# Kernel tuning notes

Measured on AMD Instinct MI355X. Metric: run time of the kernel, lower is better.

The kernel has to match this reference:

```python
import jax, jax.numpy as jnp
import numpy as np

A = -0.75  # bicubic kernel coefficient (matches torch/TF bicubic)

def _cubic_weights(t):
    """Cubic-convolution weights for the 4 taps at offsets -1,0,1,2; t in [0,1)."""
    def w_in(s):   # |s| <= 1
        return ((A + 2.0) * s - (A + 3.0)) * s * s + 1.0
    def w_out(s):  # 1 < |s| < 2
        return ((A * s - 5.0 * A) * s + 8.0 * A) * s - 4.0 * A
    return jnp.stack([w_out(t + 1.0), w_in(t), w_in(1.0 - t), w_out(2.0 - t)], axis=-1)

def setup_inputs() -> dict:
    key = jax.random.key(0)
    k1, k2 = jax.random.split(key)
    B, Hf, Wf, C = 8, 160, 160, 64
    H, W = 1280, 1280
    x = jax.random.normal(k1, (B, Hf, Wf, C), dtype=jnp.float32)
    # keypoint positions in original-image pixel coords [0, W-1] x [0, H-1]
    u = jax.random.uniform(k2, (B, 4096, 2), dtype=jnp.float32)
    pos = u * jnp.array([W - 1, H - 1], dtype=jnp.float32)
    return {"x": x, "pos": pos, "H": H, "W": W}

def reference(x, pos, H, W):
    """Bicubic grid_sample at sparse positions; align_corners=False, zeros padding.
    x: [B,Hf,Wf,C], pos: [B,N,2] (x,y) in original HxW pixel coords -> [B,N,C]."""
    B, Hf, Wf, C = x.shape
    # normalize to [-1,1] using the ORIGINAL resolution (H, W)
    gx = 2.0 * pos[..., 0] / (W - 1) - 1.0
    gy = 2.0 * pos[..., 1] / (H - 1) - 1.0
    # unnormalize to feature-map coords (align_corners=False)
    ix = ((gx + 1.0) * Wf - 1.0) * 0.5
    iy = ((gy + 1.0) * Hf - 1.0) * 0.5
    fx = jnp.floor(ix); fy = jnp.floor(iy)
    tx = ix - fx; ty = iy - fy
    offs = jnp.arange(-1, 3, dtype=jnp.int32)            # 4 taps
    xi = fx.astype(jnp.int32)[..., None] + offs           # [B,N,4]
    yi = fy.astype(jnp.int32)[..., None] + offs           # [B,N,4]
    wx = _cubic_weights(tx)                                # [B,N,4]
    wy = _cubic_weights(ty)                                # [B,N,4]
    # zeros padding: mask out-of-bounds taps
    vx = (xi >= 0) & (xi < Wf)
    vy = (yi >= 0) & (yi < Hf)
    xc = jnp.clip(xi, 0, Wf - 1)
    yc = jnp.clip(yi, 0, Hf - 1)
    lin = yc[:, :, :, None] * Wf + xc[:, :, None, :]       # [B,N,4,4] (i=y tap, j=x tap)
    xflat = x.reshape(B, Hf * Wf, C)
    vals = jax.vmap(lambda xb, ib: xb[ib])(xflat, lin)     # [B,N,4,4,C]
    m = (vy[:, :, :, None] & vx[:, :, None, :]).astype(x.dtype)
    vals = vals * m[..., None]
    return jnp.einsum('bnijc,bni,bnj->bnc', vals, wy, wx)  # [B,N,C]
```

## Files before the change

kernel.cpp:

```cpp
#include <hip/hip_runtime.h>
#include <hip/hip_bf16.h>

constexpr int B  = 8;
constexpr int Hf = 160;
constexpr int Wf = 160;
constexpr int C  = 64;
constexpr int N  = 4096;
constexpr int NXCD = 8;

typedef float f32x4 __attribute__((ext_vector_type(4)));
typedef float f32x2 __attribute__((ext_vector_type(2)));

__device__ __forceinline__ void cubic_weights(float t, float w[4]) {
    const float A = -0.75f;
    float s;
    s = t + 1.0f;
    w[0] = ((A * s - 5.0f * A) * s + 8.0f * A) * s - 4.0f * A;
    s = t;
    w[1] = ((A + 2.0f) * s - (A + 3.0f)) * s * s + 1.0f;
    s = 1.0f - t;
    w[2] = ((A + 2.0f) * s - (A + 3.0f)) * s * s + 1.0f;
    s = 2.0f - t;
    w[3] = ((A * s - 5.0f * A) * s + 8.0f * A) * s - 4.0f * A;
}

__global__ __launch_bounds__(256)
void interp_sparse_bicubic(const float* __restrict__ x,
                           const float* __restrict__ pos,
                           const int* __restrict__ Hp,
                           const int* __restrict__ Wp,
                           float* __restrict__ out) {
    int blk  = blockIdx.x;
    int b    = blk & (NXCD - 1);
    int slot = blk >> 3;
    int q    = threadIdx.x & 15;
    int pib  = threadIdx.x >> 4;
    int n    = slot * 16 + pib;
    int pnt  = b * N + n;

    f32x2 p = *reinterpret_cast<const f32x2*>(pos + (size_t)pnt * 2);
    float Wo = (float)Wp[0];
    float Ho = (float)Hp[0];

    float gx = 2.0f * p.x / (Wo - 1.0f) - 1.0f;
    float gy = 2.0f * p.y / (Ho - 1.0f) - 1.0f;
    float ix = ((gx + 1.0f) * (float)Wf - 1.0f) * 0.5f;
    float iy = ((gy + 1.0f) * (float)Hf - 1.0f) * 0.5f;

    float fx = floorf(ix), fy = floorf(iy);
    float tx = ix - fx,    ty = iy - fy;
    int x0 = (int)fx, y0 = (int)fy;

    float wx[4], wy[4];
    cubic_weights(tx, wx);
    cubic_weights(ty, wy);

    int yc[4], xc[4];
    #pragma unroll
    for (int i = 0; i < 4; ++i) {
        int yi = y0 - 1 + i;
        wy[i] = (yi >= 0 && yi < Hf) ? wy[i] : 0.0f;
        yc[i] = min(max(yi, 0), Hf - 1);
        int xj = x0 - 1 + i;
        wx[i] = (xj >= 0 && xj < Wf) ? wx[i] : 0.0f;
        xc[i] = min(max(xj, 0), Wf - 1);
    }

    const float* xb = x + (size_t)b * (Hf * Wf * C) + q * 4;

    f32x4 v[4][4];
    #pragma unroll
    for (int i = 0; i < 4; ++i) {
        const float* row = xb + (size_t)yc[i] * (Wf * C);
        #pragma unroll
        for (int j = 0; j < 4; ++j) {
            v[i][j] = *reinterpret_cast<const f32x4*>(row + (size_t)xc[j] * C);
        }
    }

    f32x4 acc = {0.f, 0.f, 0.f, 0.f};
    #pragma unroll
    for (int i = 0; i < 4; ++i) {
        #pragma unroll
        for (int j = 0; j < 4; ++j) {
            float w = wy[i] * wx[j];
            acc.x = fmaf(w, v[i][j].x, acc.x);
            acc.y = fmaf(w, v[i][j].y, acc.y);
            acc.z = fmaf(w, v[i][j].z, acc.z);
            acc.w = fmaf(w, v[i][j].w, acc.w);
        }
    }

    f32x4* op = reinterpret_cast<f32x4*>(out + (size_t)pnt * C + q * 4);
    __builtin_nontemporal_store(acc, op);
}

extern "C" void kernel_launch(void* const* d_in, const int* in_sizes, int n_in,
                              void* d_out, int out_size, void* d_ws, size_t ws_size,
                              hipStream_t stream) {
    const float* x   = (const float*)d_in[0];
    const float* pos = (const float*)d_in[1];
    const int*   Hp  = (const int*)d_in[2];
    const int*   Wp  = (const int*)d_in[3];
    float* out = (float*)d_out;

    int grid = B * (N / 16);
    interp_sparse_bicubic<<<grid, 256, 0, stream>>>(x, pos, Hp, Wp, out);
}
```

Baseline: 14.76 us.

## Bin keypoints into spatial tiles so blocks share cached feature neighborhoods

Adds a pre-pass that buckets each keypoint by its 13x13 feature-map tile, using atomic counters in the workspace and an overflow list for crowded bins. The interpolation kernel then processes one bin per block, so the points a block handles read overlapping 4x4 neighborhoods and get better cache reuse. This costs an extra memset and an extra kernel launch, uneven per-block work, and gather-indexed reads of pos and writes of out. If the workspace is too small, the original direct kernel is used instead.

Result: slower. 27.01 us (+83.0%).

```diff
diff --git a/kernel.cpp b/kernel.cpp
--- a/kernel.cpp
+++ b/kernel.cpp
@@ -7,6 +7,15 @@
 constexpr int C  = 64;
 constexpr int N  = 4096;
 constexpr int NXCD = 8;
+
+constexpr int TILE = 13;
+constexpr int TPS  = 13;
+constexpr int BINS = TPS * TPS;
+constexpr int CAP  = 64;
+constexpr int OBLK = 64;
+constexpr int CNTS = BINS + 1;
+
+constexpr size_t WS_NEED = (size_t)(B * CNTS + B * BINS * CAP + B * N) * 4;
 
 typedef float f32x4 __attribute__((ext_vector_type(4)));
 typedef float f32x2 __attribute__((ext_vector_type(2)));
@@ -24,23 +33,11 @@
     w[3] = ((A * s - 5.0f * A) * s + 8.0f * A) * s - 4.0f * A;
 }
 
-__global__ __launch_bounds__(256)
-void interp_sparse_bicubic(const float* __restrict__ x,
-                           const float* __restrict__ pos,
-                           const int* __restrict__ Hp,
-                           const int* __restrict__ Wp,
-                           float* __restrict__ out) {
-    int blk  = blockIdx.x;
-    int b    = blk & (NXCD - 1);
-    int slot = blk >> 3;
-    int q    = threadIdx.x & 15;
-    int pib  = threadIdx.x >> 4;
-    int n    = slot * 16 + pib;
-    int pnt  = b * N + n;
-
+__device__ __forceinline__ void eval_point(const float* __restrict__ xb,
+                                           const float* __restrict__ pos,
+                                           float* __restrict__ out,
+                                           int pnt, int q, float Wo, float Ho) {
     f32x2 p = *reinterpret_cast<const f32x2*>(pos + (size_t)pnt * 2);
-    float Wo = (float)Wp[0];
-    float Ho = (float)Hp[0];
 
     float gx = 2.0f * p.x / (Wo - 1.0f) - 1.0f;
     float gy = 2.0f * p.y / (Ho - 1.0f) - 1.0f;
@@ -66,16 +63,13 @@
         xc[i] = min(max(xj, 0), Wf - 1);
     }
 
-    const float* xb = x + (size_t)b * (Hf * Wf * C) + q * 4;
-
     f32x4 v[4][4];
     #pragma unroll
     for (int i = 0; i < 4; ++i) {
         const float* row = xb + (size_t)yc[i] * (Wf * C);
         #pragma unroll
-        for (int j = 0; j < 4; ++j) {
+        for (int j = 0; j < 4; ++j)
             v[i][j] = *reinterpret_cast<const f32x4*>(row + (size_t)xc[j] * C);
-        }
     }
 
     f32x4 acc = {0.f, 0.f, 0.f, 0.f};
@@ -95,6 +89,92 @@
     __builtin_nontemporal_store(acc, op);
 }
 
+__global__ __launch_bounds__(256)
+void bin_points(const float* __restrict__ pos, const int* __restrict__ Hp,
+                const int* __restrict__ Wp, int* __restrict__ ws) {
+    int pid = blockIdx.x * blockDim.x + threadIdx.x;
+    if (pid >= B * N) return;
+    int b = pid / N, n = pid - b * N;
+
+    f32x2 p = *reinterpret_cast<const f32x2*>(pos + (size_t)pid * 2);
+    float Wo = (float)Wp[0], Ho = (float)Hp[0];
+    float gx = 2.0f * p.x / (Wo - 1.0f) - 1.0f;
+    float gy = 2.0f * p.y / (Ho - 1.0f) - 1.0f;
+    float ix = ((gx + 1.0f) * (float)Wf - 1.0f) * 0.5f;
+    float iy = ((gy + 1.0f) * (float)Hf - 1.0f) * 0.5f;
+    int x0 = min(max((int)floorf(ix), 0), Wf - 1);
+    int y0 = min(max((int)floorf(iy), 0), Hf - 1);
+    int bin = (y0 / TILE) * TPS + (x0 / TILE);
+
+    int* cnt    = ws;
+    int* bucket = ws + B * CNTS;
+    int* ovf    = bucket + B * BINS * CAP;
+
+    int slot = atomicAdd(&cnt[b * CNTS + bin], 1);
+    if (slot < CAP) {
+        bucket[((size_t)b * BINS + bin) * CAP + slot] = n;
+    } else {
+        int os = atomicAdd(&cnt[b * CNTS + BINS], 1);
+        ovf[b * N + os] = n;
+    }
+}
+
+__global__ __launch_bounds__(256)
+void interp_binned(const float* __restrict__ x, const float* __restrict__ pos,
+                   const int* __restrict__ Hp, const int* __restrict__ Wp,
+                   const int* __restrict__ ws, float* __restrict__ out) {
+    int g = blockIdx.x;
+    int b = g & (NXCD - 1);
+    int u = g >> 3;
+
+    const int* cnt    = ws;
+    const int* bucket = ws + B * CNTS;
+    const int* ovf    = bucket + B * BINS * CAP;
+
+    int q   = threadIdx.x & 15;
+    int pib = threadIdx.x >> 4;
+    float Wo = (float)Wp[0], Ho = (float)Hp[0];
+    const float* xb = x + (size_t)b * (Hf * Wf * C) + q * 4;
+
+    if (u < BINS) {
+        int cv = cnt[b * CNTS + u];
+        int m  = min(cv, CAP);
+        const int* list = bucket + ((size_t)b * BINS + u) * CAP;
+        for (int base = 0; base < m; base += 16) {
+            int i = base + pib;
+            if (i < m) {
+                int n = list[i];
+                eval_point(xb, pos, out, b * N + n, q, Wo, Ho);
+            }
+        }
+    } else {
+        int j  = u - BINS;
+        int ov = cnt[b * CNTS + BINS];
+        for (int base = j * 16; base < ov; base += OBLK * 16) {
+            int i = base + pib;
+            if (i < ov) {
+                int n = ovf[b * N + i];
+                eval_point(xb, pos, out, b * N + n, q, Wo, Ho);
+            }
+        }
+    }
+}
+
+__global__ __launch_bounds__(256)
+void interp_direct(const float* __restrict__ x, const float* __restrict__ pos,
+                   const int* __restrict__ Hp, const int* __restrict__ Wp,
+                   float* __restrict__ out) {
+    int blk  = blockIdx.x;
+    int b    = blk & (NXCD - 1);
+    int slot = blk >> 3;
+    int q    = threadIdx.x & 15;
+    int pib  = threadIdx.x >> 4;
+    int pnt  = b * N + slot * 16 + pib;
+    float Wo = (float)Wp[0], Ho = (float)Hp[0];
+    const float* xb = x + (size_t)b * (Hf * Wf * C) + q * 4;
+    eval_point(xb, pos, out, pnt, q, Wo, Ho);
+}
+
 extern "C" void kernel_launch(void* const* d_in, const int* in_sizes, int n_in,
                               void* d_out, int out_size, void* d_ws, size_t ws_size,
                               hipStream_t stream) {
@@ -104,6 +184,17 @@
     const int*   Wp  = (const int*)d_in[3];
     float* out = (float*)d_out;
 
-    int grid = B * (N / 16);
-    interp_sparse_bicubic<<<grid, 256, 0, stream>>>(x, pos, Hp, Wp, out);
-}
+    if (ws_size < WS_NEED) {
+        int grid = B * (N / 16);
+        interp_direct<<<grid, 256, 0, stream>>>(x, pos, Hp, Wp, out);
+        return;
+    }
+
+    int* ws = (int*)d_ws;
+    hipMemsetAsync(ws, 0, (size_t)B * CNTS * sizeof(int), stream);
+
+    bin_points<<<(B * N + 255) / 256, 256, 0, stream>>>(pos, Hp, Wp, ws);
+
+    int grid = B * (BINS + OBLK);
+    interp_binned<<<grid, 256, 0, stream>>>(x, pos, Hp, Wp, ws, out);
+}
```

## Convert feature map to bf16 in workspace before sparse bicubic gather

Applied to the files above, without the earlier changes.

Adds a pre-pass kernel that converts the full fp32 feature map to bf16 in the workspace. The interpolation kernel then gathers half-width taps and accumulates in fp32. This aims to halve the bytes fetched by the 16-tap gather. In exchange it adds a full read and write pass over the whole feature map on every call, plus bf16 rounding error. It falls back to the direct fp32 kernel when the workspace is too small.

Result: slower. 23.86 us (+61.7%).

```diff
diff --git a/kernel.cpp b/kernel.cpp
--- a/kernel.cpp
+++ b/kernel.cpp
@@ -8,8 +8,24 @@
 constexpr int N  = 4096;
 constexpr int NXCD = 8;
 
-typedef float f32x4 __attribute__((ext_vector_type(4)));
-typedef float f32x2 __attribute__((ext_vector_type(2)));
+constexpr size_t WS_NEED = (size_t)B * Hf * Wf * C * 2;
+
+typedef float    f32x4  __attribute__((ext_vector_type(4)));
+typedef float    f32x2  __attribute__((ext_vector_type(2)));
+typedef unsigned short u16x8 __attribute__((ext_vector_type(8)));
+typedef unsigned int   u32x2 __attribute__((ext_vector_type(2)));
+
+__device__ __forceinline__ unsigned short f2bf_rne(float f) {
+    unsigned int u = __builtin_bit_cast(unsigned int, f);
+    u = (u + 0x7fffu + ((u >> 16) & 1u)) >> 16;
+    return (unsigned short)u;
+}
+__device__ __forceinline__ float bf_lo(unsigned int w) {
+    return __builtin_bit_cast(float, w << 16);
+}
+__device__ __forceinline__ float bf_hi(unsigned int w) {
+    return __builtin_bit_cast(float, w & 0xffff0000u);
+}
 
 __device__ __forceinline__ void cubic_weights(float t, float w[4]) {
     const float A = -0.75f;
@@ -25,22 +41,36 @@
 }
 
 __global__ __launch_bounds__(256)
-void interp_sparse_bicubic(const float* __restrict__ x,
-                           const float* __restrict__ pos,
-                           const int* __restrict__ Hp,
-                           const int* __restrict__ Wp,
-                           float* __restrict__ out) {
+void convert_bf16(const float* __restrict__ x, unsigned short* __restrict__ xh) {
+    int blk  = blockIdx.x;
+    int b    = blk & (NXCD - 1);
+    int slot = blk >> 3;
+    size_t base = (size_t)b * (Hf * Wf * C)
+                + (size_t)slot * (256 * 8) + (size_t)threadIdx.x * 8;
+    const f32x4* src = reinterpret_cast<const f32x4*>(x + base);
+    f32x4 a = src[0], c = src[1];
+    u16x8 o;
+    o[0] = f2bf_rne(a.x); o[1] = f2bf_rne(a.y);
+    o[2] = f2bf_rne(a.z); o[3] = f2bf_rne(a.w);
+    o[4] = f2bf_rne(c.x); o[5] = f2bf_rne(c.y);
+    o[6] = f2bf_rne(c.z); o[7] = f2bf_rne(c.w);
+    *reinterpret_cast<u16x8*>(xh + base) = o;
+}
+
+__global__ __launch_bounds__(256)
+void interp_bf16(const unsigned short* __restrict__ xh,
+                 const float* __restrict__ pos,
+                 const int* __restrict__ Hp, const int* __restrict__ Wp,
+                 float* __restrict__ out) {
     int blk  = blockIdx.x;
     int b    = blk & (NXCD - 1);
     int slot = blk >> 3;
     int q    = threadIdx.x & 15;
     int pib  = threadIdx.x >> 4;
-    int n    = slot * 16 + pib;
-    int pnt  = b * N + n;
+    int pnt  = b * N + slot * 16 + pib;
 
     f32x2 p = *reinterpret_cast<const f32x2*>(pos + (size_t)pnt * 2);
-    float Wo = (float)Wp[0];
-    float Ho = (float)Hp[0];
+    float Wo = (float)Wp[0], Ho = (float)Hp[0];
 
     float gx = 2.0f * p.x / (Wo - 1.0f) - 1.0f;
     float gy = 2.0f * p.y / (Ho - 1.0f) - 1.0f;
@@ -66,18 +96,83 @@
         xc[i] = min(max(xj, 0), Wf - 1);
     }
 
+    const unsigned short* xb = xh + (size_t)b * (Hf * Wf * C) + q * 4;
+
+    u32x2 v[4][4];
+    #pragma unroll
+    for (int i = 0; i < 4; ++i) {
+        const unsigned short* row = xb + (size_t)yc[i] * (Wf * C);
+        #pragma unroll
+        for (int j = 0; j < 4; ++j)
+            v[i][j] = *reinterpret_cast<const u32x2*>(row + (size_t)xc[j] * C);
+    }
+
+    float a0 = 0.f, a1 = 0.f, a2 = 0.f, a3 = 0.f;
+    #pragma unroll
+    for (int i = 0; i < 4; ++i) {
+        #pragma unroll
+        for (int j = 0; j < 4; ++j) {
+            float w = wy[i] * wx[j];
+            unsigned int lo = v[i][j].x, hi = v[i][j].y;
+            a0 = fmaf(w, bf_lo(lo), a0);
+            a1 = fmaf(w, bf_hi(lo), a1);
+            a2 = fmaf(w, bf_lo(hi), a2);
+            a3 = fmaf(w, bf_hi(hi), a3);
+        }
+    }
+
+    f32x4 acc = {a0, a1, a2, a3};
+    f32x4* op = reinterpret_cast<f32x4*>(out + (size_t)pnt * C + q * 4);
+    __builtin_nontemporal_store(acc, op);
+}
+
+__global__ __launch_bounds__(256)
+void interp_direct(const float* __restrict__ x, const float* __restrict__ pos,
+                   const int* __restrict__ Hp, const int* __restrict__ Wp,
+                   float* __restrict__ out) {
+    int blk  = blockIdx.x;
+    int b    = blk & (NXCD - 1);
+    int slot = blk >> 3;
+    int q    = threadIdx.x & 15;
+    int pib  = threadIdx.x >> 4;
+    int pnt  = b * N + slot * 16 + pib;
+
+    f32x2 p = *reinterpret_cast<const f32x2*>(pos + (size_t)pnt * 2);
+    float Wo = (float)Wp[0], Ho = (float)Hp[0];
+
+    float gx = 2.0f * p.x / (Wo - 1.0f) - 1.0f;
+    float gy = 2.0f * p.y / (Ho - 1.0f) - 1.0f;
+    float ix = ((gx + 1.0f) * (float)Wf - 1.0f) * 0.5f;
+    float iy = ((gy + 1.0f) * (float)Hf - 1.0f) * 0.5f;
+
+    float fx = floorf(ix), fy = floorf(iy);
+    float tx = ix - fx,    ty = iy - fy;
+    int x0 = (int)fx, y0 = (int)fy;
+
+    float wx[4], wy[4];
+    cubic_weights(tx, wx);
+    cubic_weights(ty, wy);
+
+    int yc[4], xc[4];
+    #pragma unroll
+    for (int i = 0; i < 4; ++i) {
+        int yi = y0 - 1 + i;
+        wy[i] = (yi >= 0 && yi < Hf) ? wy[i] : 0.0f;
+        yc[i] = min(max(yi, 0), Hf - 1);
+        int xj = x0 - 1 + i;
+        wx[i] = (xj >= 0 && xj < Wf) ? wx[i] : 0.0f;
+        xc[i] = min(max(xj, 0), Wf - 1);
+    }
+
     const float* xb = x + (size_t)b * (Hf * Wf * C) + q * 4;
-
     f32x4 v[4][4];
     #pragma unroll
     for (int i = 0; i < 4; ++i) {
         const float* row = xb + (size_t)yc[i] * (Wf * C);
         #pragma unroll
-        for (int j = 0; j < 4; ++j) {
+        for (int j = 0; j < 4; ++j)
             v[i][j] = *reinterpret_cast<const f32x4*>(row + (size_t)xc[j] * C);
-        }
-    }
-
+    }
     f32x4 acc = {0.f, 0.f, 0.f, 0.f};
     #pragma unroll
     for (int i = 0; i < 4; ++i) {
@@ -90,7 +185,6 @@
             acc.w = fmaf(w, v[i][j].w, acc.w);
         }
     }
-
     f32x4* op = reinterpret_cast<f32x4*>(out + (size_t)pnt * C + q * 4);
     __builtin_nontemporal_store(acc, op);
 }
@@ -104,6 +198,12 @@
     const int*   Wp  = (const int*)d_in[3];
     float* out = (float*)d_out;
 
-    int grid = B * (N / 16);
-    interp_sparse_bicubic<<<grid, 256, 0, stream>>>(x, pos, Hp, Wp, out);
-}
+    if (ws_size < WS_NEED) {
+        interp_direct<<<B * (N / 16), 256, 0, stream>>>(x, pos, Hp, Wp, out);
+        return;
+    }
+
+    unsigned short* xh = (unsigned short*)d_ws;
+    convert_bf16<<<B * (Hf * Wf * C / (256 * 8)), 256, 0, stream>>>(x, xh);
+    interp_bf16<<<B * (N / 16), 256, 0, stream>>>(xh, pos, Hp, Wp, out);
+}
```

## Split channels into halves per XCD so each XCD's L2 holds less feature data

Applied to the files above, without the earlier changes.

Blocks are remapped so each of the 8 XCD slots handles a pair of batches and one half of the channels (32 floats), with 8 threads per point and 32 points per block. Previously each XCD owned one whole batch image of features. The new mapping keeps the per-XCD working set the same size but splits each gather row into half-width 128-byte segments. The likely intent is better L2 hit behaviour or finer memory granularity, at the cost of shorter contiguous reads per tap and duplicated index and weight computation for each channel half.

Measured after the change: 14.94 us. No clear change (+1.2%).

```diff
diff --git a/kernel.cpp b/kernel.cpp
--- a/kernel.cpp
+++ b/kernel.cpp
@@ -6,7 +6,6 @@
 constexpr int Wf = 160;
 constexpr int C  = 64;
 constexpr int N  = 4096;
-constexpr int NXCD = 8;
 
 typedef float f32x4 __attribute__((ext_vector_type(4)));
 typedef float f32x2 __attribute__((ext_vector_type(2)));
@@ -25,22 +24,23 @@
 }
 
 __global__ __launch_bounds__(256)
-void interp_sparse_bicubic(const float* __restrict__ x,
-                           const float* __restrict__ pos,
-                           const int* __restrict__ Hp,
-                           const int* __restrict__ Wp,
-                           float* __restrict__ out) {
-    int blk  = blockIdx.x;
-    int b    = blk & (NXCD - 1);
-    int slot = blk >> 3;
-    int q    = threadIdx.x & 15;
-    int pib  = threadIdx.x >> 4;
-    int n    = slot * 16 + pib;
+void interp_sliced(const float* __restrict__ x, const float* __restrict__ pos,
+                   const int* __restrict__ Hp, const int* __restrict__ Wp,
+                   float* __restrict__ out) {
+    int g    = blockIdx.x;
+    int s    = g & 7;
+    int pair = s >> 1;
+    int h    = s & 1;
+    int slot = g >> 3;
+    int q    = threadIdx.x & 7;
+    int pib  = threadIdx.x >> 3;
+    int pp   = slot * 32 + pib;
+    int b    = pair * 2 + (pp >> 12);
+    int n    = pp & (N - 1);
     int pnt  = b * N + n;
 
     f32x2 p = *reinterpret_cast<const f32x2*>(pos + (size_t)pnt * 2);
-    float Wo = (float)Wp[0];
-    float Ho = (float)Hp[0];
+    float Wo = (float)Wp[0], Ho = (float)Hp[0];
 
     float gx = 2.0f * p.x / (Wo - 1.0f) - 1.0f;
     float gy = 2.0f * p.y / (Ho - 1.0f) - 1.0f;
@@ -66,16 +66,16 @@
         xc[i] = min(max(xj, 0), Wf - 1);
     }
 
-    const float* xb = x + (size_t)b * (Hf * Wf * C) + q * 4;
+    int ch = h * 32 + q * 4;
+    const float* xb = x + (size_t)b * (Hf * Wf * C) + ch;
 
     f32x4 v[4][4];
     #pragma unroll
     for (int i = 0; i < 4; ++i) {
         const float* row = xb + (size_t)yc[i] * (Wf * C);
         #pragma unroll
-        for (int j = 0; j < 4; ++j) {
+        for (int j = 0; j < 4; ++j)
             v[i][j] = *reinterpret_cast<const f32x4*>(row + (size_t)xc[j] * C);
-        }
     }
 
     f32x4 acc = {0.f, 0.f, 0.f, 0.f};
@@ -91,7 +91,7 @@
         }
     }
 
-    f32x4* op = reinterpret_cast<f32x4*>(out + (size_t)pnt * C + q * 4);
+    f32x4* op = reinterpret_cast<f32x4*>(out + (size_t)pnt * C + ch);
     __builtin_nontemporal_store(acc, op);
 }
 
@@ -104,6 +104,5 @@
     const int*   Wp  = (const int*)d_in[3];
     float* out = (float*)d_out;
 
-    int grid = B * (N / 16);
-    interp_sparse_bicubic<<<grid, 256, 0, stream>>>(x, pos, Hp, Wp, out);
+    interp_sliced<<<2048, 256, 0, stream>>>(x, pos, Hp, Wp, out);
 }
```
